# Kernel optimization log

Hardware: AMD Instinct MI355X
Metric: run time of the kernel (lower is better)

The kernel has to match this reference:

```python
import jax, jax.numpy as jnp
import numpy as np

D_MODEL = 768
D_FF = 2048
N_EXP = 8
TOP_K = 2


def setup_inputs() -> dict:
    key = jax.random.key(0)
    ks = jax.random.split(key, 8)
    s = 0.02
    inputs = jax.random.normal(ks[0], (4, 2048, D_MODEL), dtype=jnp.float32)
    gate_w = jax.random.normal(ks[1], (D_MODEL, N_EXP), dtype=jnp.float32) * s
    w1 = jax.random.normal(ks[2], (N_EXP, D_MODEL, D_FF), dtype=jnp.float32) * s
    w3 = jax.random.normal(ks[3], (N_EXP, D_MODEL, D_FF), dtype=jnp.float32) * s
    w2 = jax.random.normal(ks[4], (N_EXP, D_FF, D_MODEL), dtype=jnp.float32) * s
    sw1 = jax.random.normal(ks[5], (D_MODEL, D_FF), dtype=jnp.float32) * s
    sw3 = jax.random.normal(ks[6], (D_MODEL, D_FF), dtype=jnp.float32) * s
    sw2 = jax.random.normal(ks[7], (D_FF, D_MODEL), dtype=jnp.float32) * s
    return {"inputs": inputs, "gate_w": gate_w, "w1": w1, "w3": w3, "w2": w2,
            "sw1": sw1, "sw3": sw3, "sw2": sw2}


def _swiglu(x, wa, wb, wc):
    # silu(x @ wa) * (x @ wb) @ wc
    return (jax.nn.silu(x @ wa) * (x @ wb)) @ wc


def reference(inputs, gate_w, w1, w3, w2, sw1, sw3, sw2):
    B, T, D = inputs.shape
    x = inputs.reshape(-1, D)                      # [N, D], N = B*T
    logits = x @ gate_w                            # [N, E]
    topk_scores, topk_idx = jax.lax.top_k(logits, TOP_K)  # [N, K]
    probs = jax.nn.softmax(topk_scores.astype(jnp.float32), axis=-1).astype(inputs.dtype)
    # per-token per-expert combine weight: [N, E]
    one_hot = jax.nn.one_hot(topk_idx, N_EXP, dtype=probs.dtype)  # [N, K, E]
    comb = jnp.einsum('nk,nke->ne', probs, one_hot)               # [N, E]
    out = jnp.zeros_like(x)
    for e in range(N_EXP):  # fixed small expert loop
        out = out + comb[:, e:e + 1] * _swiglu(x, w1[e], w3[e], w2[e])
    out = out + _swiglu(x, sw1, sw3, sw2)
    return out.reshape(B, T, D)
```

## Files before the change

kernel.cpp:

```cpp
#include <hip/hip_runtime.h>
#include <hip/hip_bf16.h>

#define N_TOK 8192
#define DM 768
#define DFF 2048
#define NE 8
#define SHARED_BASE 17408
#define TOTAL_ROWS 25600

typedef __attribute__((ext_vector_type(8))) __bf16 bf16x8;
typedef __attribute__((ext_vector_type(4))) float f32x4;

__device__ __forceinline__ unsigned short f2bf(float f) {
  union { float f; unsigned u; } a; a.f = f;
  unsigned r = a.u + 0x7FFFu + ((a.u >> 16) & 1u);
  return (unsigned short)(r >> 16);
}

__device__ __forceinline__ void gload16(const void* g, void* l) {
  __builtin_amdgcn_global_load_lds((const __attribute__((address_space(1))) void*)g,
                                   (__attribute__((address_space(3))) void*)l, 16, 0, 0);
}


__global__ void cvt_x_kernel(const float4* __restrict__ src, ushort4* __restrict__ dst, int n4) {
  int stride = gridDim.x * blockDim.x;
  for (int i = blockIdx.x * blockDim.x + threadIdx.x; i < n4; i += stride) {
    float4 v = src[i];
    ushort4 o;
    o.x = f2bf(v.x); o.y = f2bf(v.y); o.z = f2bf(v.z); o.w = f2bf(v.w);
    dst[i] = o;
  }
}

__global__ void transpose_all_kernel(
    const float* __restrict__ w1, const float* __restrict__ w3, const float* __restrict__ w2,
    const float* __restrict__ sw1, const float* __restrict__ sw3, const float* __restrict__ sw2,
    unsigned short* __restrict__ w1T, unsigned short* __restrict__ w3T,
    unsigned short* __restrict__ w2T,
    unsigned short* __restrict__ sw1T, unsigned short* __restrict__ sw3T,
    unsigned short* __restrict__ sw2T) {
  __shared__ float tile[64][65];
  const int z = blockIdx.z;
  const float* s; unsigned short* d; int R, C;
  if (z < 8)       { s = w1 + (size_t)z * DM * DFF;        d = w1T + (size_t)z * DM * DFF;        R = DM;  C = DFF; }
  else if (z < 16) { s = w3 + (size_t)(z - 8) * DM * DFF;  d = w3T + (size_t)(z - 8) * DM * DFF;  R = DM;  C = DFF; }
  else if (z < 24) { s = w2 + (size_t)(z - 16) * DFF * DM; d = w2T + (size_t)(z - 16) * DFF * DM; R = DFF; C = DM;  }
  else if (z == 24){ s = sw1; d = sw1T; R = DM;  C = DFF; }
  else if (z == 25){ s = sw3; d = sw3T; R = DM;  C = DFF; }
  else             { s = sw2; d = sw2T; R = DFF; C = DM;  }
  int c0 = blockIdx.x * 64, r0 = blockIdx.y * 64;
  if (c0 >= C || r0 >= R) return;
  int tx = threadIdx.x & 63, ty = threadIdx.x >> 6;
#pragma unroll
  for (int i = 0; i < 16; i++) {
    int row = i * 4 + ty;
    tile[row][tx] = s[(size_t)(r0 + row) * C + c0 + tx];
  }
  __syncthreads();
#pragma unroll
  for (int i = 0; i < 16; i++) {
    int row = i * 4 + ty;
    d[(size_t)(c0 + row) * R + r0 + tx] = f2bf(tile[tx][row]);
  }
}

__global__ __launch_bounds__(256) void gate_kernel(
    const float* __restrict__ x, const float* __restrict__ gw,
    float* __restrict__ probs, int* __restrict__ idxo) {
  __shared__ float gws[8][768];
  const int tid = threadIdx.x;
  for (int i = tid; i < DM * 2; i += 256) {
    float4 v = ((const float4*)gw)[i];
    int dd = i >> 1;
    int e0 = (i & 1) * 4;
    gws[e0 + 0][dd] = v.x; gws[e0 + 1][dd] = v.y;
    gws[e0 + 2][dd] = v.z; gws[e0 + 3][dd] = v.w;
  }
  __syncthreads();
  const int lane = tid & 63, wv = tid >> 6;
  const int tok0 = blockIdx.x * 16 + wv * 4;
  for (int i = 0; i < 4; i++) {
    const int n = tok0 + i;
    const float* xr = x + (size_t)n * DM;
    float xv[12];
#pragma unroll
    for (int it = 0; it < 12; it++) xv[it] = xr[it * 64 + lane];
    double acc[8];
#pragma unroll
    for (int e = 0; e < 8; e++) {
      double a = 0.0;
#pragma unroll
      for (int it = 0; it < 12; it++) a += (double)xv[it] * (double)gws[e][it * 64 + lane];
      acc[e] = a;
    }
#pragma unroll
    for (int off = 32; off > 0; off >>= 1)
#pragma unroll
      for (int e = 0; e < 8; e++) acc[e] += __shfl_xor(acc[e], off);
    if (lane == 0) {
      int e0 = 0; double v0 = acc[0];
#pragma unroll
      for (int e = 1; e < 8; e++) if (acc[e] > v0) { v0 = acc[e]; e0 = e; }
      int e1 = -1; double v1 = -1e300;
#pragma unroll
      for (int e = 0; e < 8; e++) if (e != e0 && acc[e] > v1) { v1 = acc[e]; e1 = e; }
      double p0 = 1.0 / (1.0 + exp(v1 - v0));
      probs[n * 2 + 0] = (float)p0;
      probs[n * 2 + 1] = (float)(1.0 - p0);
      idxo[n * 2 + 0] = e0;
      idxo[n * 2 + 1] = e1;
    }
  }
}

__global__ __launch_bounds__(256) void route_kernel(
    const int* __restrict__ idxo,
    int* __restrict__ cnt, int* __restrict__ offs,
    int* __restrict__ list, int* __restrict__ slt) {
  __shared__ int lcnt[256][8];
  __shared__ int lstart[256][8];
  __shared__ int base[8];
  const int t = threadIdx.x;
#pragma unroll
  for (int e = 0; e < 8; e++) lcnt[t][e] = 0;
  __syncthreads();
  const int i0 = t * 64;
  for (int j = 0; j < 64; j++) {
    int e = idxo[i0 + j];
    lcnt[t][e]++;
  }
  __syncthreads();
  if (t < 8) {
    int run = 0;
    for (int tt = 0; tt < 256; tt++) { lstart[tt][t] = run; run += lcnt[tt][t]; }
    base[t] = run;
  }
  __syncthreads();
  if (t == 0) {
    int cum = 0;
    for (int e = 0; e < 8; e++) {
      int tot = base[e];
      cnt[e] = tot; offs[e] = cum;
      base[e] = cum;
      cum += (tot + 127) & ~127;
    }
    offs[8] = cum;
  }
  __syncthreads();
#pragma unroll
  for (int e = 0; e < 8; e++) lcnt[t][e] = base[e] + lstart[t][e];
  for (int j = 0; j < 64; j++) {
    int i = i0 + j;
    int e = idxo[i];
    int pos = lcnt[t][e]++;
    list[pos] = i >> 1;
    slt[i] = pos;
  }
}

__global__ __launch_bounds__(256, 2) void gemm1_kernel(
    const char* __restrict__ xb,
    const char* __restrict__ w1T,
    const char* __restrict__ w3T,
    const char* __restrict__ sw1T,
    const char* __restrict__ sw3T,
    const int* __restrict__ list, const int* __restrict__ cnt, const int* __restrict__ offs,
    unsigned short* __restrict__ Hb)
{
  __shared__ unsigned short Al[128 * 64];
  __shared__ unsigned short B1l[64 * 64];
  __shared__ unsigned short B3l[64 * 64];

  const int by = blockIdx.y;
  const int f0 = blockIdx.x * 64;
  const int tid = threadIdx.x;
  const int lane = tid & 63;
  const int wv = tid >> 6;
  const int wm = wv >> 1, wn = wv & 1;
  const int wflat = tid & ~63;

  const char *w1p, *w3p;
  int base_slot, tbase, cnt_e, offs_e = 0;
  const bool is_shared = (by >= 512);
  if (!is_shared) {
    int e = by >> 6, t = by & 63;
    cnt_e = cnt[e];
    if (t * 128 >= cnt_e) return;
    offs_e = offs[e];
    base_slot = offs_e + t * 128;
    tbase = t * 128;
    w1p = w1T + (size_t)e * DFF * DM * 2;
    w3p = w3T + (size_t)e * DFF * DM * 2;
  } else {
    int t = by - 512;
    base_slot = SHARED_BASE + t * 128;
    tbase = t * 128;
    cnt_e = 1 << 30;
    w1p = sw1T; w3p = sw3T;
  }

  const int brow = tid >> 3;
  const int bcol = tid & 7;

  size_t abase[4];
#pragma unroll
  for (int it = 0; it < 4; it++) {
    int row = it * 32 + brow;
    int tok;
    if (is_shared) tok = tbase + row;
    else {
      int ie = tbase + row;
      if (ie >= cnt_e) ie = cnt_e - 1;
      tok = list[offs_e + ie];
    }
    abase[it] = (size_t)tok * (DM * 2) + (size_t)((bcol ^ (row & 7)) << 4);
  }
  size_t bbase[2];
#pragma unroll
  for (int it = 0; it < 2; it++) {
    int row = it * 32 + brow;
    bbase[it] = (size_t)(f0 + row) * (DM * 2) + (size_t)((bcol ^ (row & 7)) << 4);
  }

  f32x4 acc1[4][2], acc3[4][2];
  const f32x4 z4 = {0.f, 0.f, 0.f, 0.f};
#pragma unroll
  for (int mi = 0; mi < 4; mi++)
#pragma unroll
    for (int ni = 0; ni < 2; ni++) { acc1[mi][ni] = z4; acc3[mi][ni] = z4; }

  const int ml = lane & 15, kg = lane >> 4;

  for (int ks = 0; ks < 12; ks++) {
#pragma unroll
    for (int it = 0; it < 4; it++)
      gload16(xb + abase[it] + ks * 128, (char*)Al + (size_t)((it * 256 + wflat) * 16));
#pragma unroll
    for (int it = 0; it < 2; it++) {
      gload16(w1p + bbase[it] + ks * 128, (char*)B1l + (size_t)((it * 256 + wflat) * 16));
      gload16(w3p + bbase[it] + ks * 128, (char*)B3l + (size_t)((it * 256 + wflat) * 16));
    }
    __syncthreads();
#pragma unroll
    for (int kk = 0; kk < 2; kk++) {
      const int kblk = kk * 4 + kg;
      bf16x8 af[4], b1f[2], b3f[2];
#pragma unroll
      for (int mi = 0; mi < 4; mi++) {
        int m = wm * 64 + mi * 16 + ml;
        af[mi] = *(const bf16x8*)((const char*)Al + m * 128 + ((kblk ^ (ml & 7)) << 4));
      }
#pragma unroll
      for (int ni = 0; ni < 2; ni++) {
        int nn = wn * 32 + ni * 16 + ml;
        int boff = nn * 128 + ((kblk ^ (ml & 7)) << 4);
        b1f[ni] = *(const bf16x8*)((const char*)B1l + boff);
        b3f[ni] = *(const bf16x8*)((const char*)B3l + boff);
      }
#pragma unroll
      for (int mi = 0; mi < 4; mi++)
#pragma unroll
        for (int ni = 0; ni < 2; ni++) {
          acc1[mi][ni] = __builtin_amdgcn_mfma_f32_16x16x32_bf16(af[mi], b1f[ni], acc1[mi][ni], 0, 0, 0);
          acc3[mi][ni] = __builtin_amdgcn_mfma_f32_16x16x32_bf16(af[mi], b3f[ni], acc3[mi][ni], 0, 0, 0);
        }
    }
    __syncthreads();
  }

#pragma unroll
  for (int mi = 0; mi < 4; mi++) {
#pragma unroll
    for (int ni = 0; ni < 2; ni++) {
#pragma unroll
      for (int r = 0; r < 4; r++) {
        int row = wm * 64 + mi * 16 + (lane >> 4) * 4 + r;
        int col = f0 + wn * 32 + ni * 16 + ml;
        float h1 = acc1[mi][ni][r], h3 = acc3[mi][ni][r];
        float s = h1 / (1.0f + expf(-h1));
        Hb[(size_t)(base_slot + row) * DFF + col] = f2bf(s * h3);
      }
    }
  }
}

__global__ __launch_bounds__(512, 4) void gemm2_kernel(
    const char* __restrict__ Hb,
    const char* __restrict__ w2T,
    const char* __restrict__ sw2T,
    const int* __restrict__ cnt, const int* __restrict__ offs,
    float* __restrict__ Ob,
    float* __restrict__ out)
{
  __shared__ unsigned short Al[128 * 64];
  __shared__ unsigned short Bl[256 * 64];

  const int by = blockIdx.y;
  const int d0 = blockIdx.x * 256;
  const int tid = threadIdx.x;
  const int lane = tid & 63;
  const int wv = tid >> 6;
  const int wm = wv >> 2;
  const int wn = wv & 3;
  const int wflat = tid & ~63;

  const char* w2p;
  int base_slot, tbase, cnt_e;
  const bool is_shared = (by >= 512);
  if (!is_shared) {
    int e = by >> 6, t = by & 63;
    cnt_e = cnt[e];
    if (t * 128 >= cnt_e) return;
    base_slot = offs[e] + t * 128;
    tbase = t * 128;
    w2p = w2T + (size_t)e * DM * DFF * 2;
  } else {
    int t = by - 512;
    base_slot = SHARED_BASE + t * 128;
    tbase = t * 128;
    cnt_e = 1 << 30;
    w2p = sw2T;
  }

  const int brow = tid >> 3, bcol = tid & 7;
  size_t abase[2], bbase[4];
#pragma unroll
  for (int it = 0; it < 2; it++) {
    int row = it * 64 + brow;
    abase[it] = (size_t)(base_slot + row) * (DFF * 2) + (size_t)((bcol ^ (row & 7)) << 4);
  }
#pragma unroll
  for (int it = 0; it < 4; it++) {
    int row = it * 64 + brow;
    bbase[it] = (size_t)(d0 + row) * (DFF * 2) + (size_t)((bcol ^ (row & 7)) << 4);
  }

  f32x4 acc[4][4];
  const f32x4 z4 = {0.f, 0.f, 0.f, 0.f};
#pragma unroll
  for (int mi = 0; mi < 4; mi++)
#pragma unroll
    for (int nj = 0; nj < 4; nj++) acc[mi][nj] = z4;

  const int ml = lane & 15, kg = lane >> 4;

  for (int ks = 0; ks < 32; ks++) {
#pragma unroll
    for (int it = 0; it < 2; it++)
      gload16(Hb + abase[it] + ks * 128, (char*)Al + (size_t)((it * 512 + tid) * 16));
#pragma unroll
    for (int it = 0; it < 4; it++)
      gload16(w2p + bbase[it] + ks * 128, (char*)Bl + (size_t)((it * 512 + tid) * 16));
    __syncthreads();
#pragma unroll
    for (int kk = 0; kk < 2; kk++) {
      const int kblk = kk * 4 + kg;
      bf16x8 af[4], bfr[4];
#pragma unroll
      for (int mi = 0; mi < 4; mi++) {
        int m = wm * 64 + mi * 16 + ml;
        af[mi] = *(const bf16x8*)((const char*)Al + m * 128 + ((kblk ^ (ml & 7)) << 4));
      }
#pragma unroll
      for (int nj = 0; nj < 4; nj++) {
        int nn = wn * 64 + nj * 16 + ml;
        bfr[nj] = *(const bf16x8*)((const char*)Bl + nn * 128 + ((kblk ^ (ml & 7)) << 4));
      }
#pragma unroll
      for (int mi = 0; mi < 4; mi++)
#pragma unroll
        for (int nj = 0; nj < 4; nj++)
          acc[mi][nj] = __builtin_amdgcn_mfma_f32_16x16x32_bf16(af[mi], bfr[nj], acc[mi][nj], 0, 0, 0);
    }
    __syncthreads();
  }

#pragma unroll
  for (int mi = 0; mi < 4; mi++) {
#pragma unroll
    for (int r = 0; r < 4; r++) {
      int row = wm * 64 + mi * 16 + (lane >> 4) * 4 + r;
      float* orow = is_shared ? (out + (size_t)(tbase + row) * DM + d0)
                              : (Ob + (size_t)(base_slot + row) * DM + d0);
#pragma unroll
      for (int nj = 0; nj < 4; nj++)
        orow[wn * 64 + nj * 16 + ml] = acc[mi][nj][r];
    }
  }
}

__global__ __launch_bounds__(192) void combine_kernel(
    const float4* __restrict__ Ob4, const int* __restrict__ slt,
    const float* __restrict__ probs, float4* __restrict__ out4) {
  const int n = blockIdx.x;
  const int t = threadIdx.x;
  const int s0 = slt[2 * n], s1 = slt[2 * n + 1];
  const float p0 = probs[2 * n], p1 = probs[2 * n + 1];
  float4 a = out4[(size_t)n * 192 + t];
  float4 b = Ob4[(size_t)s0 * 192 + t];
  float4 c = Ob4[(size_t)s1 * 192 + t];
  a.x += p0 * b.x + p1 * c.x;
  a.y += p0 * b.y + p1 * c.y;
  a.z += p0 * b.z + p1 * c.z;
  a.w += p0 * b.w + p1 * c.w;
  out4[(size_t)n * 192 + t] = a;
}


extern "C" void kernel_launch(void* const* d_in, const int* in_sizes, int n_in,
                              void* d_out, int out_size, void* d_ws, size_t ws_size,
                              hipStream_t stream) {
  const float* x   = (const float*)d_in[0];
  const float* gw  = (const float*)d_in[1];
  const float* w1  = (const float*)d_in[2];
  const float* w3  = (const float*)d_in[3];
  const float* w2  = (const float*)d_in[4];
  const float* sw1 = (const float*)d_in[5];
  const float* sw3 = (const float*)d_in[6];
  const float* sw2 = (const float*)d_in[7];
  float* out = (float*)d_out;
  char* ws = (char*)d_ws;

  char* xb   = ws;
  char* w2T  = xb + 12582912;
  char* sw2T = w2T + 25165824;
  char* U    = sw2T + 3145728;
  char* w1T  = U;
  char* w3T  = w1T + 25165824;
  char* sw1T = w3T + 25165824;
  char* sw3T = sw1T + 3145728;
  char* Ob   = U;
  char* Hb   = U + 56623104;
  char* probs= Hb + 104857600;
  char* idxo = probs + 65536;
  char* lst  = idxo + 65536;
  char* slt  = lst + 69632;
  char* cntb = slt + 69632;
  char* offb = cntb + 64;

  cvt_x_kernel<<<2048, 256, 0, stream>>>((const float4*)x, (ushort4*)xb, N_TOK * DM / 4);
  transpose_all_kernel<<<dim3(32, 32, 27), 256, 0, stream>>>(
      w1, w3, w2, sw1, sw3, sw2,
      (unsigned short*)w1T, (unsigned short*)w3T, (unsigned short*)w2T,
      (unsigned short*)sw1T, (unsigned short*)sw3T, (unsigned short*)sw2T);

  gate_kernel<<<512, 256, 0, stream>>>(x, gw, (float*)probs, (int*)idxo);
  route_kernel<<<1, 256, 0, stream>>>((const int*)idxo,
                                      (int*)cntb, (int*)offb, (int*)lst, (int*)slt);

  gemm1_kernel<<<dim3(32, 576), 256, 0, stream>>>(xb, w1T, w3T, sw1T, sw3T,
      (const int*)lst, (const int*)cntb, (const int*)offb, (unsigned short*)Hb);

  gemm2_kernel<<<dim3(3, 576), 512, 0, stream>>>(Hb, w2T, sw2T,
      (const int*)cntb, (const int*)offb, (float*)Ob, out);

  combine_kernel<<<N_TOK, 192, 0, stream>>>((const float4*)Ob, (const int*)slt,
                                            (const float*)probs, (float4*)out);
}
```

Measured before the change: 390.1 us.

## Widen gemm1 tile, fuse x conversion into gate, store expert outputs in bf16

gemm1 moves to 512-thread blocks with a 128x128 tile that interleaves w1 and w3 columns in one shared B buffer, which halves the grid and raises A-tile reuse. The separate x-to-bf16 conversion kernel is folded into the gate kernel. The transpose kernel now writes pairs of bf16 values per store. Routed expert outputs are written as bf16 instead of fp32, cutting intermediate traffic in gemm2 and combine at some cost in precision.

```diff
diff --git a/kernel.cpp b/kernel.cpp
--- a/kernel.cpp
+++ b/kernel.cpp
@@ -17,21 +17,15 @@
   return (unsigned short)(r >> 16);
 }
 
+__device__ __forceinline__ float bfu(unsigned short u) {
+  union { unsigned u; float f; } x; x.u = (unsigned)u << 16; return x.f;
+}
+
 __device__ __forceinline__ void gload16(const void* g, void* l) {
   __builtin_amdgcn_global_load_lds((const __attribute__((address_space(1))) void*)g,
                                    (__attribute__((address_space(3))) void*)l, 16, 0, 0);
 }
 
-
-__global__ void cvt_x_kernel(const float4* __restrict__ src, ushort4* __restrict__ dst, int n4) {
-  int stride = gridDim.x * blockDim.x;
-  for (int i = blockIdx.x * blockDim.x + threadIdx.x; i < n4; i += stride) {
-    float4 v = src[i];
-    ushort4 o;
-    o.x = f2bf(v.x); o.y = f2bf(v.y); o.z = f2bf(v.z); o.w = f2bf(v.w);
-    dst[i] = o;
-  }
-}
 
 __global__ void transpose_all_kernel(
     const float* __restrict__ w1, const float* __restrict__ w3, const float* __restrict__ w2,
@@ -58,16 +52,20 @@
     tile[row][tx] = s[(size_t)(r0 + row) * C + c0 + tx];
   }
   __syncthreads();
-#pragma unroll
-  for (int i = 0; i < 16; i++) {
-    int row = i * 4 + ty;
-    d[(size_t)(c0 + row) * R + r0 + tx] = f2bf(tile[tx][row]);
+  int tx2 = threadIdx.x & 31, ty8 = threadIdx.x >> 5;
+#pragma unroll
+  for (int i = 0; i < 8; i++) {
+    int row = i * 8 + ty8;
+    ushort2 v;
+    v.x = f2bf(tile[tx2 * 2][row]);
+    v.y = f2bf(tile[tx2 * 2 + 1][row]);
+    *(ushort2*)&d[(size_t)(c0 + row) * R + r0 + tx2 * 2] = v;
   }
 }
 
 __global__ __launch_bounds__(256) void gate_kernel(
     const float* __restrict__ x, const float* __restrict__ gw,
-    float* __restrict__ probs, int* __restrict__ idxo) {
+    float* __restrict__ probs, int* __restrict__ idxo, unsigned short* __restrict__ xb) {
   __shared__ float gws[8][768];
   const int tid = threadIdx.x;
   for (int i = tid; i < DM * 2; i += 256) {
@@ -86,6 +84,8 @@
     float xv[12];
 #pragma unroll
     for (int it = 0; it < 12; it++) xv[it] = xr[it * 64 + lane];
+#pragma unroll
+    for (int it = 0; it < 12; it++) xb[(size_t)n * DM + it * 64 + lane] = f2bf(xv[it]);
     double acc[8];
 #pragma unroll
     for (int e = 0; e < 8; e++) {
@@ -159,7 +159,7 @@
   }
 }
 
-__global__ __launch_bounds__(256, 2) void gemm1_kernel(
+__global__ __launch_bounds__(512, 4) void gemm1_kernel(
     const char* __restrict__ xb,
     const char* __restrict__ w1T,
     const char* __restrict__ w3T,
@@ -169,16 +169,16 @@
     unsigned short* __restrict__ Hb)
 {
   __shared__ unsigned short Al[128 * 64];
-  __shared__ unsigned short B1l[64 * 64];
-  __shared__ unsigned short B3l[64 * 64];
+  __shared__ unsigned short Bl[256 * 64];
 
   const int by = blockIdx.y;
-  const int f0 = blockIdx.x * 64;
+  const int f0 = blockIdx.x * 128;
   const int tid = threadIdx.x;
   const int lane = tid & 63;
   const int wv = tid >> 6;
-  const int wm = wv >> 1, wn = wv & 1;
-  const int wflat = tid & ~63;
+  const int wm = wv >> 2;
+  const int wn = wv & 3;
+  const int ml = lane & 15, kg = lane >> 4;
 
   const char *w1p, *w3p;
   int base_slot, tbase, cnt_e, offs_e = 0;
@@ -200,13 +200,13 @@
     w1p = sw1T; w3p = sw3T;
   }
 
-  const int brow = tid >> 3;
-  const int bcol = tid & 7;
-
-  size_t abase[4];
-#pragma unroll
-  for (int it = 0; it < 4; it++) {
-    int row = it * 32 + brow;
+  const int srow = tid >> 3;
+  const int schk = tid & 7;
+
+  size_t abase[2];
+#pragma unroll
+  for (int it = 0; it < 2; it++) {
+    int row = it * 64 + srow;
     int tok;
     if (is_shared) tok = tbase + row;
     else {
@@ -214,57 +214,54 @@
       if (ie >= cnt_e) ie = cnt_e - 1;
       tok = list[offs_e + ie];
     }
-    abase[it] = (size_t)tok * (DM * 2) + (size_t)((bcol ^ (row & 7)) << 4);
-  }
-  size_t bbase[2];
-#pragma unroll
-  for (int it = 0; it < 2; it++) {
-    int row = it * 32 + brow;
-    bbase[it] = (size_t)(f0 + row) * (DM * 2) + (size_t)((bcol ^ (row & 7)) << 4);
-  }
-
-  f32x4 acc1[4][2], acc3[4][2];
+    abase[it] = (size_t)tok * (DM * 2) + (size_t)((schk ^ (row & 7)) << 4);
+  }
+  const char* bsrc[4];
+#pragma unroll
+  for (int it = 0; it < 4; it++) {
+    int row = it * 64 + srow;
+    int wn_r = row >> 6;
+    int w = row & 63;
+    int mat = w >> 5;
+    int f = f0 + wn_r * 32 + (w & 31);
+    bsrc[it] = (mat ? w3p : w1p) + (size_t)f * (DM * 2) + (size_t)((schk ^ (row & 7)) << 4);
+  }
+
+  f32x4 acc[4][4];
   const f32x4 z4 = {0.f, 0.f, 0.f, 0.f};
 #pragma unroll
   for (int mi = 0; mi < 4; mi++)
 #pragma unroll
-    for (int ni = 0; ni < 2; ni++) { acc1[mi][ni] = z4; acc3[mi][ni] = z4; }
-
-  const int ml = lane & 15, kg = lane >> 4;
+    for (int nj = 0; nj < 4; nj++) acc[mi][nj] = z4;
 
   for (int ks = 0; ks < 12; ks++) {
 #pragma unroll
+    for (int it = 0; it < 2; it++)
+      gload16(xb + abase[it] + ks * 128, (char*)Al + (size_t)((it * 512 + tid) * 16));
+#pragma unroll
     for (int it = 0; it < 4; it++)
-      gload16(xb + abase[it] + ks * 128, (char*)Al + (size_t)((it * 256 + wflat) * 16));
-#pragma unroll
-    for (int it = 0; it < 2; it++) {
-      gload16(w1p + bbase[it] + ks * 128, (char*)B1l + (size_t)((it * 256 + wflat) * 16));
-      gload16(w3p + bbase[it] + ks * 128, (char*)B3l + (size_t)((it * 256 + wflat) * 16));
-    }
+      gload16(bsrc[it] + ks * 128, (char*)Bl + (size_t)((it * 512 + tid) * 16));
     __syncthreads();
 #pragma unroll
     for (int kk = 0; kk < 2; kk++) {
       const int kblk = kk * 4 + kg;
-      bf16x8 af[4], b1f[2], b3f[2];
+      const int chk = (kblk ^ (ml & 7)) << 4;
+      bf16x8 af[4], bfr[4];
 #pragma unroll
       for (int mi = 0; mi < 4; mi++) {
         int m = wm * 64 + mi * 16 + ml;
-        af[mi] = *(const bf16x8*)((const char*)Al + m * 128 + ((kblk ^ (ml & 7)) << 4));
-      }
-#pragma unroll
-      for (int ni = 0; ni < 2; ni++) {
-        int nn = wn * 32 + ni * 16 + ml;
-        int boff = nn * 128 + ((kblk ^ (ml & 7)) << 4);
-        b1f[ni] = *(const bf16x8*)((const char*)B1l + boff);
-        b3f[ni] = *(const bf16x8*)((const char*)B3l + boff);
+        af[mi] = *(const bf16x8*)((const char*)Al + m * 128 + chk);
+      }
+#pragma unroll
+      for (int nj = 0; nj < 4; nj++) {
+        int nn = wn * 64 + nj * 16 + ml;
+        bfr[nj] = *(const bf16x8*)((const char*)Bl + nn * 128 + chk);
       }
 #pragma unroll
       for (int mi = 0; mi < 4; mi++)
 #pragma unroll
-        for (int ni = 0; ni < 2; ni++) {
-          acc1[mi][ni] = __builtin_amdgcn_mfma_f32_16x16x32_bf16(af[mi], b1f[ni], acc1[mi][ni], 0, 0, 0);
-          acc3[mi][ni] = __builtin_amdgcn_mfma_f32_16x16x32_bf16(af[mi], b3f[ni], acc3[mi][ni], 0, 0, 0);
-        }
+        for (int nj = 0; nj < 4; nj++)
+          acc[mi][nj] = __builtin_amdgcn_mfma_f32_16x16x32_bf16(af[mi], bfr[nj], acc[mi][nj], 0, 0, 0);
     }
     __syncthreads();
   }
@@ -272,14 +269,14 @@
 #pragma unroll
   for (int mi = 0; mi < 4; mi++) {
 #pragma unroll
-    for (int ni = 0; ni < 2; ni++) {
-#pragma unroll
-      for (int r = 0; r < 4; r++) {
-        int row = wm * 64 + mi * 16 + (lane >> 4) * 4 + r;
-        int col = f0 + wn * 32 + ni * 16 + ml;
-        float h1 = acc1[mi][ni][r], h3 = acc3[mi][ni][r];
+    for (int r = 0; r < 4; r++) {
+      int row = wm * 64 + mi * 16 + (lane >> 4) * 4 + r;
+      size_t hrow = (size_t)(base_slot + row) * DFF;
+#pragma unroll
+      for (int nj = 0; nj < 2; nj++) {
+        float h1 = acc[mi][nj][r], h3 = acc[mi][nj + 2][r];
         float s = h1 / (1.0f + expf(-h1));
-        Hb[(size_t)(base_slot + row) * DFF + col] = f2bf(s * h3);
+        Hb[hrow + f0 + wn * 32 + nj * 16 + ml] = f2bf(s * h3);
       }
     }
   }
@@ -290,7 +287,7 @@
     const char* __restrict__ w2T,
     const char* __restrict__ sw2T,
     const int* __restrict__ cnt, const int* __restrict__ offs,
-    float* __restrict__ Ob,
+    unsigned short* __restrict__ Obh,
     float* __restrict__ out)
 {
   __shared__ unsigned short Al[128 * 64];
@@ -303,7 +300,7 @@
   const int wv = tid >> 6;
   const int wm = wv >> 2;
   const int wn = wv & 3;
-  const int wflat = tid & ~63;
+  const int ml = lane & 15, kg = lane >> 4;
 
   const char* w2p;
   int base_slot, tbase, cnt_e;
@@ -323,17 +320,18 @@
     w2p = sw2T;
   }
 
-  const int brow = tid >> 3, bcol = tid & 7;
-  size_t abase[2], bbase[4];
+  const int srow = tid >> 3, schk = tid & 7;
+  size_t abase[2];
 #pragma unroll
   for (int it = 0; it < 2; it++) {
-    int row = it * 64 + brow;
-    abase[it] = (size_t)(base_slot + row) * (DFF * 2) + (size_t)((bcol ^ (row & 7)) << 4);
-  }
+    int row = it * 64 + srow;
+    abase[it] = (size_t)(base_slot + row) * (DFF * 2) + (size_t)((schk ^ (row & 7)) << 4);
+  }
+  size_t bbase[4];
 #pragma unroll
   for (int it = 0; it < 4; it++) {
-    int row = it * 64 + brow;
-    bbase[it] = (size_t)(d0 + row) * (DFF * 2) + (size_t)((bcol ^ (row & 7)) << 4);
+    int row = it * 64 + srow;
+    bbase[it] = (size_t)(d0 + row) * (DFF * 2) + (size_t)((schk ^ (row & 7)) << 4);
   }
 
   f32x4 acc[4][4];
@@ -342,8 +340,6 @@
   for (int mi = 0; mi < 4; mi++)
 #pragma unroll
     for (int nj = 0; nj < 4; nj++) acc[mi][nj] = z4;
-
-  const int ml = lane & 15, kg = lane >> 4;
 
   for (int ks = 0; ks < 32; ks++) {
 #pragma unroll
@@ -356,16 +352,17 @@
 #pragma unroll
     for (int kk = 0; kk < 2; kk++) {
       const int kblk = kk * 4 + kg;
+      const int chk = (kblk ^ (ml & 7)) << 4;
       bf16x8 af[4], bfr[4];
 #pragma unroll
       for (int mi = 0; mi < 4; mi++) {
         int m = wm * 64 + mi * 16 + ml;
-        af[mi] = *(const bf16x8*)((const char*)Al + m * 128 + ((kblk ^ (ml & 7)) << 4));
+        af[mi] = *(const bf16x8*)((const char*)Al + m * 128 + chk);
       }
 #pragma unroll
       for (int nj = 0; nj < 4; nj++) {
         int nn = wn * 64 + nj * 16 + ml;
-        bfr[nj] = *(const bf16x8*)((const char*)Bl + nn * 128 + ((kblk ^ (ml & 7)) << 4));
+        bfr[nj] = *(const bf16x8*)((const char*)Bl + nn * 128 + chk);
       }
 #pragma unroll
       for (int mi = 0; mi < 4; mi++)
@@ -381,29 +378,35 @@
 #pragma unroll
     for (int r = 0; r < 4; r++) {
       int row = wm * 64 + mi * 16 + (lane >> 4) * 4 + r;
-      float* orow = is_shared ? (out + (size_t)(tbase + row) * DM + d0)
-                              : (Ob + (size_t)(base_slot + row) * DM + d0);
-#pragma unroll
-      for (int nj = 0; nj < 4; nj++)
-        orow[wn * 64 + nj * 16 + ml] = acc[mi][nj][r];
+      if (is_shared) {
+        float* orow = out + (size_t)(tbase + row) * DM + d0;
+#pragma unroll
+        for (int nj = 0; nj < 4; nj++)
+          orow[wn * 64 + nj * 16 + ml] = acc[mi][nj][r];
+      } else {
+        unsigned short* orow = Obh + (size_t)(base_slot + row) * DM + d0;
+#pragma unroll
+        for (int nj = 0; nj < 4; nj++)
+          orow[wn * 64 + nj * 16 + ml] = f2bf(acc[mi][nj][r]);
+      }
     }
   }
 }
 
 __global__ __launch_bounds__(192) void combine_kernel(
-    const float4* __restrict__ Ob4, const int* __restrict__ slt,
+    const unsigned short* __restrict__ Obh, const int* __restrict__ slt,
     const float* __restrict__ probs, float4* __restrict__ out4) {
   const int n = blockIdx.x;
   const int t = threadIdx.x;
   const int s0 = slt[2 * n], s1 = slt[2 * n + 1];
   const float p0 = probs[2 * n], p1 = probs[2 * n + 1];
+  ushort4 b4 = *(const ushort4*)(Obh + (size_t)s0 * DM + t * 4);
+  ushort4 c4 = *(const ushort4*)(Obh + (size_t)s1 * DM + t * 4);
   float4 a = out4[(size_t)n * 192 + t];
-  float4 b = Ob4[(size_t)s0 * 192 + t];
-  float4 c = Ob4[(size_t)s1 * 192 + t];
-  a.x += p0 * b.x + p1 * c.x;
-  a.y += p0 * b.y + p1 * c.y;
-  a.z += p0 * b.z + p1 * c.z;
-  a.w += p0 * b.w + p1 * c.w;
+  a.x += p0 * bfu(b4.x) + p1 * bfu(c4.x);
+  a.y += p0 * bfu(b4.y) + p1 * bfu(c4.y);
+  a.z += p0 * bfu(b4.z) + p1 * bfu(c4.z);
+  a.w += p0 * bfu(b4.w) + p1 * bfu(c4.w);
   out4[(size_t)n * 192 + t] = a;
 }
 
@@ -439,22 +442,21 @@
   char* cntb = slt + 69632;
   char* offb = cntb + 64;
 
-  cvt_x_kernel<<<2048, 256, 0, stream>>>((const float4*)x, (ushort4*)xb, N_TOK * DM / 4);
   transpose_all_kernel<<<dim3(32, 32, 27), 256, 0, stream>>>(
       w1, w3, w2, sw1, sw3, sw2,
       (unsigned short*)w1T, (unsigned short*)w3T, (unsigned short*)w2T,
       (unsigned short*)sw1T, (unsigned short*)sw3T, (unsigned short*)sw2T);
 
-  gate_kernel<<<512, 256, 0, stream>>>(x, gw, (float*)probs, (int*)idxo);
+  gate_kernel<<<512, 256, 0, stream>>>(x, gw, (float*)probs, (int*)idxo, (unsigned short*)xb);
   route_kernel<<<1, 256, 0, stream>>>((const int*)idxo,
                                       (int*)cntb, (int*)offb, (int*)lst, (int*)slt);
 
-  gemm1_kernel<<<dim3(32, 576), 256, 0, stream>>>(xb, w1T, w3T, sw1T, sw3T,
+  gemm1_kernel<<<dim3(16, 576), 512, 0, stream>>>(xb, w1T, w3T, sw1T, sw3T,
       (const int*)lst, (const int*)cntb, (const int*)offb, (unsigned short*)Hb);
 
   gemm2_kernel<<<dim3(3, 576), 512, 0, stream>>>(Hb, w2T, sw2T,
-      (const int*)cntb, (const int*)offb, (float*)Ob, out);
-
-  combine_kernel<<<N_TOK, 192, 0, stream>>>((const float4*)Ob, (const int*)slt,
+      (const int*)cntb, (const int*)offb, (unsigned short*)Ob, out);
+
+  combine_kernel<<<N_TOK, 192, 0, stream>>>((const unsigned short*)Ob, (const int*)slt,
                                             (const float*)probs, (float4*)out);
 }
```

Result: no change. 395.4 us (+1.4%).
